# Kernel optimization log

Measured on AMD Instinct MI355X. Metric: run time of the kernel, lower is better.

The kernel has to match this reference:

```python
import jax, jax.numpy as jnp
import numpy as np

L = 512
Z_DIM = 128
C = 128
EPS = 1e-5


def _ln(x, g, b):
    m = jnp.mean(x, axis=-1, keepdims=True)
    v = jnp.var(x, axis=-1, keepdims=True)
    return (x - m) * jax.lax.rsqrt(v + EPS) * g + b


def setup_inputs() -> dict:
    key = jax.random.key(0)
    ks = jax.random.split(key, 12)
    s_z = 1.0 / np.sqrt(Z_DIM)
    s_c = 1.0 / np.sqrt(C)
    return {
        "z": jax.random.normal(ks[0], (L, L, Z_DIM), dtype=jnp.float32),
        "norm_g": jnp.ones((Z_DIM,), jnp.float32),
        "norm_b": jnp.zeros((Z_DIM,), jnp.float32),
        "a_w": jax.random.normal(ks[1], (C, Z_DIM), jnp.float32) * s_z,
        "a_b": jnp.zeros((C,), jnp.float32),
        "ag_w": jax.random.normal(ks[2], (C, Z_DIM), jnp.float32) * s_z,
        "ag_b": jnp.zeros((C,), jnp.float32),
        "onorm_g": jnp.ones((C,), jnp.float32),
        "onorm_b": jnp.zeros((C,), jnp.float32),
        "o_w": jax.random.normal(ks[3], (Z_DIM, C), jnp.float32) * s_c,
        "o_b": jnp.zeros((Z_DIM,), jnp.float32),
        "g_w": jax.random.normal(ks[4], (Z_DIM, Z_DIM), jnp.float32) * s_z,
        "g_b": jnp.zeros((Z_DIM,), jnp.float32),
    }


def reference(z, norm_g, norm_b, a_w, a_b, ag_w, ag_b, onorm_g, onorm_b, o_w, o_b, g_w, g_b):
    zn = _ln(z, norm_g, norm_b)                                   # [L, L, z_dim]
    # gated projection; source computes b identically to a (alinear/aglinear for both)
    a = (zn @ a_w.T + a_b) * jax.nn.sigmoid(zn @ ag_w.T + ag_b)   # [L, L, c]
    o = jnp.einsum('ilc,jlc->ijc', a, a)                          # [L, L, c]
    o = _ln(o, onorm_g, onorm_b)
    o = o @ o_w.T + o_b                                           # [L, L, z_dim]
    return o * jax.nn.sigmoid(zn @ g_w.T + g_b)
```

## Files before the change

### kernel.cpp

```cpp
#include <hip/hip_runtime.h>
#include <stdint.h>

typedef unsigned short bf16;
typedef __attribute__((ext_vector_type(8))) short short8;
typedef __attribute__((ext_vector_type(4))) float f32x4;

#define MFMA16(a, b, c) __builtin_amdgcn_mfma_f32_16x16x32_bf16((a), (b), (c), 0, 0, 0)

__device__ __forceinline__ bf16 f2bf(float f) {
    unsigned u = __float_as_uint(f);
    u += 0x7fffu + ((u >> 16) & 1u);
    return (bf16)(u >> 16);
}
__device__ __forceinline__ float bf2f(bf16 s) { return __uint_as_float(((unsigned)s) << 16); }

__device__ __forceinline__ void gload_lds16(const void* g, void* lds) {
    auto gp = (const __attribute__((address_space(1))) unsigned int*)(uintptr_t)g;
    auto lp = (__attribute__((address_space(3))) unsigned int*)(uintptr_t)lds;
    __builtin_amdgcn_global_load_lds(gp, lp, 16, 0, 0);
}

__global__ __launch_bounds__(256) void k_wconv(const float* __restrict__ aw,
                                               const float* __restrict__ agw,
                                               const float* __restrict__ gw,
                                               const float* __restrict__ ow,
                                               bf16* __restrict__ wbf,
                                               bf16* __restrict__ owbf) {
    int i = blockIdx.x * 256 + threadIdx.x;
    int m = i >> 14, k = i & 16383;
    const float* s = (m == 0) ? aw : (m == 1) ? agw : (m == 2) ? gw : ow;
    float v = s[k];
    if (m < 3) wbf[i] = f2bf(v); else owbf[k] = f2bf(v);
}

__global__ __launch_bounds__(256) void k_ln_proj(const float* __restrict__ z,
                                                 const float* __restrict__ ng,
                                                 const float* __restrict__ nb,
                                                 const float* __restrict__ ab,
                                                 const float* __restrict__ agb,
                                                 const float* __restrict__ gbv,
                                                 const bf16* __restrict__ wbf,
                                                 bf16* __restrict__ a_t,
                                                 bf16* __restrict__ gbuf) {
    __shared__ bf16 zn_s[64 * 136];
    __shared__ bf16 w_s[128 * 136];
    __shared__ float ng_s[128], nb_s[128];

    const int t = threadIdx.x;
    const int r0 = blockIdx.x * 64;
    bf16* st = w_s;

    if (t < 128) { ng_s[t] = ng[t]; nb_s[t] = nb[t]; }

    {
        int row = t >> 2, q = t & 3;
        const float* zp = z + (size_t)(r0 + row) * 128 + q * 32;
        float x[32];
        float s = 0.f, ss = 0.f;
#pragma unroll
        for (int i = 0; i < 8; ++i) {
            float4 v = ((const float4*)zp)[i];
            x[4 * i + 0] = v.x; x[4 * i + 1] = v.y; x[4 * i + 2] = v.z; x[4 * i + 3] = v.w;
        }
#pragma unroll
        for (int i = 0; i < 32; ++i) { s += x[i]; ss += x[i] * x[i]; }
        s += __shfl_xor(s, 1); ss += __shfl_xor(ss, 1);
        s += __shfl_xor(s, 2); ss += __shfl_xor(ss, 2);
        float mean = s * (1.f / 128.f);
        float var = ss * (1.f / 128.f) - mean * mean;
        float rstd = rsqrtf(var + 1e-5f);
        __syncthreads();
#pragma unroll
        for (int i = 0; i < 32; ++i) {
            int c = q * 32 + i;
            zn_s[row * 136 + c] = f2bf((x[i] - mean) * rstd * ng_s[c] + nb_s[c]);
        }
    }

    const int lane = t & 63, w = t >> 6;
    const int lr = lane & 15, quad = lane >> 4;
    const int arow = w * 16 + lr;

    auto stage_w = [&](int mat) {
        const uint4* src = (const uint4*)(wbf + mat * 16384);
#pragma unroll
        for (int i = 0; i < 8; ++i) {
            int idx = t + i * 256;
            int row = idx >> 4, part = idx & 15;
            *(uint4*)&w_s[row * 136 + part * 8] = src[idx];
        }
    };
    auto gemmv = [&](f32x4* acc) {
#pragma unroll
        for (int kk = 0; kk < 4; ++kk) {
            short8 af = *(const short8*)&zn_s[arow * 136 + kk * 32 + quad * 8];
#pragma unroll
            for (int nt = 0; nt < 8; ++nt) {
                short8 bfr = *(const short8*)&w_s[(nt * 16 + lr) * 136 + kk * 32 + quad * 8];
                acc[nt] = MFMA16(af, bfr, acc[nt]);
            }
        }
    };

    f32x4 zero4 = {0.f, 0.f, 0.f, 0.f};
    f32x4 acc_a[8], acc_b[8];
#pragma unroll
    for (int nt = 0; nt < 8; ++nt) { acc_a[nt] = zero4; acc_b[nt] = zero4; }

    stage_w(0);
    __syncthreads();
    gemmv(acc_a);
    __syncthreads();
    stage_w(1);
    __syncthreads();
    gemmv(acc_b);
    __syncthreads();

#pragma unroll
    for (int nt = 0; nt < 8; ++nt) {
        int c = nt * 16 + lr;
        float abv = ab[c], agbv = agb[c];
#pragma unroll
        for (int r = 0; r < 4; ++r) {
            int row = w * 16 + quad * 4 + r;
            float av = acc_a[nt][r] + abv;
            float agvv = acc_b[nt][r] + agbv;
            st[c * 64 + row] = f2bf(av * (1.f / (1.f + __expf(-agvv))));
        }
    }
    __syncthreads();
#pragma unroll
    for (int i = 0; i < 4; ++i) {
        int idx = t + i * 256;
        int c = idx >> 3, part = idx & 7;
        *(uint4*)(a_t + (size_t)c * 262144 + r0 + part * 8) = *(const uint4*)&st[c * 64 + part * 8];
    }
    __syncthreads();

    stage_w(2);
    __syncthreads();
#pragma unroll
    for (int nt = 0; nt < 8; ++nt) acc_a[nt] = zero4;
    gemmv(acc_a);
    __syncthreads();
#pragma unroll
    for (int nt = 0; nt < 8; ++nt) {
        int c = nt * 16 + lr;
        float gb0 = gbv[c];
#pragma unroll
        for (int r = 0; r < 4; ++r) {
            int row = w * 16 + quad * 4 + r;
            float v = acc_a[nt][r] + gb0;
            st[row * 128 + c] = f2bf(1.f / (1.f + __expf(-v)));
        }
    }
    __syncthreads();
#pragma unroll
    for (int i = 0; i < 4; ++i) {
        int idx = t + i * 256;
        int row = idx >> 4, part = idx & 15;
        *(uint4*)(gbuf + (size_t)(r0 + row) * 128 + part * 8) = *(const uint4*)&st[row * 128 + part * 8];
    }
}

__global__ __launch_bounds__(256) void k_einsum(const bf16* __restrict__ a_t,
                                                bf16* __restrict__ o_t) {
    __shared__ bf16 smem[16384];
    bf16* As = smem;
    bf16* Bs = smem + 8192;

    const int t = threadIdx.x;
    const int bx = blockIdx.x;
    const int c = bx >> 4;
    const int ti = (bx >> 2) & 3, tj = bx & 3;
    const int i0 = ti * 128, j0 = tj * 128;
    const size_t cbase = (size_t)c * 262144;
    const bf16* Ac = a_t + cbase;

    const int lane = t & 63, w = t >> 6;
    const int lr = lane & 15, quad = lane >> 4;
    const int wi = w >> 1, wj = w & 1;

    f32x4 zero4 = {0.f, 0.f, 0.f, 0.f};
    f32x4 acc[4][4];
#pragma unroll
    for (int mt = 0; mt < 4; ++mt)
#pragma unroll
        for (int nt = 0; nt < 4; ++nt) acc[mt][nt] = zero4;

    for (int kb = 0; kb < 8; ++kb) {
        __syncthreads();
#pragma unroll
        for (int q = 0; q < 4; ++q) {
            int t16 = (w << 8) + (q << 6) + lane;
            int row = t16 >> 3;
            int cb = t16 & 7;
            int cbg = cb ^ (row & 7);
            int gcol = kb * 64 + cbg * 8;
            gload_lds16(Ac + (size_t)(i0 + row) * 512 + gcol, As + (((w << 8) + (q << 6)) << 3));
            gload_lds16(Ac + (size_t)(j0 + row) * 512 + gcol, Bs + (((w << 8) + (q << 6)) << 3));
        }
        __syncthreads();
#pragma unroll
        for (int kk8 = 0; kk8 < 8; kk8 += 4) {
            short8 af[4], bfr[4];
#pragma unroll
            for (int mt = 0; mt < 4; ++mt) {
                int r = wi * 64 + mt * 16 + lr;
                af[mt] = *(const short8*)&As[r * 64 + (((kk8 + quad) ^ (lr & 7)) << 3)];
            }
#pragma unroll
            for (int nt = 0; nt < 4; ++nt) {
                int r = wj * 64 + nt * 16 + lr;
                bfr[nt] = *(const short8*)&Bs[r * 64 + (((kk8 + quad) ^ (lr & 7)) << 3)];
            }
#pragma unroll
            for (int mt = 0; mt < 4; ++mt)
#pragma unroll
                for (int nt = 0; nt < 4; ++nt)
                    acc[mt][nt] = MFMA16(af[mt], bfr[nt], acc[mt][nt]);
        }
    }

    __syncthreads();
    bf16* Cs = smem;
#pragma unroll
    for (int mt = 0; mt < 4; ++mt)
#pragma unroll
        for (int nt = 0; nt < 4; ++nt)
#pragma unroll
            for (int r = 0; r < 4; ++r) {
                int il = wi * 64 + mt * 16 + quad * 4 + r;
                int jl = wj * 64 + nt * 16 + lr;
                Cs[il * 128 + jl] = f2bf(acc[mt][nt][r]);
            }
    __syncthreads();
    bf16* Oc = o_t + cbase;
#pragma unroll
    for (int i = 0; i < 8; ++i) {
        int idx = t + (i << 8);
        int row = idx >> 4, part = idx & 15;
        *(uint4*)(Oc + (size_t)(i0 + row) * 512 + j0 + part * 8) = *(const uint4*)&Cs[row * 128 + part * 8];
    }
}

__global__ __launch_bounds__(256) void k_out(const bf16* __restrict__ o_t,
                                             const bf16* __restrict__ gbuf,
                                             const float* __restrict__ og,
                                             const float* __restrict__ ob,
                                             const bf16* __restrict__ owbf,
                                             const float* __restrict__ obias,
                                             float* __restrict__ out) {
    __shared__ bf16 pool[128 * 136];
    __shared__ float og_s[128], ob_s[128], obi_s[128];
    bf16* ot_s = pool;
    bf16* n_s = pool;

    const int t = threadIdx.x;
    const int p0 = blockIdx.x * 128;
    if (t < 128) { og_s[t] = og[t]; ob_s[t] = ob[t]; obi_s[t] = obias[t]; }

#pragma unroll
    for (int i = 0; i < 8; ++i) {
        int idx = t + (i << 8);
        int c = idx >> 4, part = idx & 15;
        *(uint4*)&ot_s[c * 128 + part * 8] = *(const uint4*)(o_t + (size_t)c * 262144 + p0 + part * 8);
    }
    __syncthreads();

    {
        int col = t >> 1, h = t & 1;
        float s = 0.f, ss = 0.f;
        float xv[64];
#pragma unroll
        for (int k = 0; k < 64; ++k) {
            float x = bf2f(ot_s[(h * 64 + k) * 128 + col]);
            xv[k] = x; s += x; ss += x * x;
        }
        s += __shfl_xor(s, 1); ss += __shfl_xor(ss, 1);
        float mean = s * (1.f / 128.f);
        float var = ss * (1.f / 128.f) - mean * mean;
        float rstd = rsqrtf(var + 1e-5f);
        __syncthreads();
#pragma unroll
        for (int k = 0; k < 64; ++k) {
            int cc = h * 64 + k;
            n_s[col * 136 + cc] = f2bf((xv[k] - mean) * rstd * og_s[cc] + ob_s[cc]);
        }
    }
    __syncthreads();

    const int lane = t & 63, w = t >> 6;
    const int lr = lane & 15, quad = lane >> 4;
    f32x4 zero4 = {0.f, 0.f, 0.f, 0.f};
    f32x4 acc[2][8];
#pragma unroll
    for (int mt = 0; mt < 2; ++mt)
#pragma unroll
        for (int nt = 0; nt < 8; ++nt) acc[mt][nt] = zero4;

#pragma unroll
    for (int kk = 0; kk < 4; ++kk) {
        short8 af[2];
#pragma unroll
        for (int mt = 0; mt < 2; ++mt)
            af[mt] = *(const short8*)&n_s[(w * 32 + mt * 16 + lr) * 136 + kk * 32 + quad * 8];
#pragma unroll
        for (int nt = 0; nt < 8; ++nt) {
            short8 bfr = *(const short8*)(owbf + (nt * 16 + lr) * 128 + kk * 32 + quad * 8);
            acc[0][nt] = MFMA16(af[0], bfr, acc[0][nt]);
            acc[1][nt] = MFMA16(af[1], bfr, acc[1][nt]);
        }
    }

#pragma unroll
    for (int mt = 0; mt < 2; ++mt)
#pragma unroll
        for (int nt = 0; nt < 8; ++nt) {
            int zd = nt * 16 + lr;
            float bias = obi_s[zd];
#pragma unroll
            for (int r = 0; r < 4; ++r) {
                int m = w * 32 + mt * 16 + quad * 4 + r;
                size_t off = (size_t)(p0 + m) * 128 + zd;
                out[off] = (acc[mt][nt][r] + bias) * bf2f(gbuf[off]);
            }
        }
}

extern "C" void kernel_launch(void* const* d_in, const int* in_sizes, int n_in,
                              void* d_out, int out_size, void* d_ws, size_t ws_size,
                              hipStream_t stream) {
    (void)in_sizes; (void)n_in; (void)out_size; (void)ws_size;
    const float* z   = (const float*)d_in[0];
    const float* ng  = (const float*)d_in[1];
    const float* nb  = (const float*)d_in[2];
    const float* aw  = (const float*)d_in[3];
    const float* ab  = (const float*)d_in[4];
    const float* agw = (const float*)d_in[5];
    const float* agb = (const float*)d_in[6];
    const float* ong = (const float*)d_in[7];
    const float* onb = (const float*)d_in[8];
    const float* ow  = (const float*)d_in[9];
    const float* obi = (const float*)d_in[10];
    const float* gw  = (const float*)d_in[11];
    const float* gbb = (const float*)d_in[12];

    char* ws = (char*)d_ws;
    bf16* wbf  = (bf16*)(ws);
    bf16* owbf = (bf16*)(ws + 98304);
    bf16* a_t  = (bf16*)(ws + 131072);
    bf16* gbuf = (bf16*)(ws + 131072 + 67108864);
    bf16* o_t  = (bf16*)(ws + 131072 + 2 * 67108864);

    k_wconv<<<256, 256, 0, stream>>>(aw, agw, gw, ow, wbf, owbf);
    k_ln_proj<<<4096, 256, 0, stream>>>(z, ng, nb, ab, agb, gbb, wbf, a_t, gbuf);
    k_einsum<<<2048, 256, 0, stream>>>(a_t, o_t);
    k_out<<<2048, 256, 0, stream>>>(o_t, gbuf, ong, onb, owbf, obi, (float*)d_out);
}
```

Baseline: 423.2 us.

## Prepack projection weights into MFMA fragment order and load them directly from global

The weight-conversion kernel now writes the three projection weights pre-permuted into the per-lane MFMA B-fragment layout. The LN/projection kernel reads those fragments straight from global (L2-resident) memory instead of staging each weight matrix through LDS with barriers. LDS use drops from about 50KB to about 34KB and several __syncthreads are removed, which should raise occupancy and cut staging overhead. The cost is more global/L2 traffic per block for weight fragments, and latency the MFMA loop has to hide.

Result: slower. 433.8 us (+2.5%).

```diff
diff --git a/kernel.cpp b/kernel.cpp
--- a/kernel.cpp
+++ b/kernel.cpp
@@ -24,13 +24,21 @@
                                                const float* __restrict__ agw,
                                                const float* __restrict__ gw,
                                                const float* __restrict__ ow,
-                                               bf16* __restrict__ wbf,
+                                               bf16* __restrict__ wpk,
                                                bf16* __restrict__ owbf) {
     int i = blockIdx.x * 256 + threadIdx.x;
-    int m = i >> 14, k = i & 16383;
-    const float* s = (m == 0) ? aw : (m == 1) ? agw : (m == 2) ? gw : ow;
-    float v = s[k];
-    if (m < 3) wbf[i] = f2bf(v); else owbf[k] = f2bf(v);
+    if (i < 49152) {
+        int m = i >> 14, r = i & 16383;
+        int kk = r >> 12, rr = r & 4095;
+        int nt = rr >> 9, li = rr & 511;
+        int lane = li >> 3, e = li & 7;
+        int lr = lane & 15, quad = lane >> 4;
+        const float* s = (m == 0) ? aw : (m == 1) ? agw : gw;
+        wpk[i] = f2bf(s[(nt * 16 + lr) * 128 + kk * 32 + quad * 8 + e]);
+    } else {
+        int k = i - 49152;
+        owbf[k] = f2bf(ow[k]);
+    }
 }
 
 __global__ __launch_bounds__(256) void k_ln_proj(const float* __restrict__ z,
@@ -39,16 +47,15 @@
                                                  const float* __restrict__ ab,
                                                  const float* __restrict__ agb,
                                                  const float* __restrict__ gbv,
-                                                 const bf16* __restrict__ wbf,
+                                                 const bf16* __restrict__ wpk,
                                                  bf16* __restrict__ a_t,
                                                  bf16* __restrict__ gbuf) {
     __shared__ bf16 zn_s[64 * 136];
-    __shared__ bf16 w_s[128 * 136];
+    __shared__ bf16 st[8192];
     __shared__ float ng_s[128], nb_s[128];
 
     const int t = threadIdx.x;
     const int r0 = blockIdx.x * 64;
-    bf16* st = w_s;
 
     if (t < 128) { ng_s[t] = ng[t]; nb_s[t] = nb[t]; }
 
@@ -76,45 +83,30 @@
             zn_s[row * 136 + c] = f2bf((x[i] - mean) * rstd * ng_s[c] + nb_s[c]);
         }
     }
+    __syncthreads();
 
     const int lane = t & 63, w = t >> 6;
     const int lr = lane & 15, quad = lane >> 4;
     const int arow = w * 16 + lr;
 
-    auto stage_w = [&](int mat) {
-        const uint4* src = (const uint4*)(wbf + mat * 16384);
-#pragma unroll
-        for (int i = 0; i < 8; ++i) {
-            int idx = t + i * 256;
-            int row = idx >> 4, part = idx & 15;
-            *(uint4*)&w_s[row * 136 + part * 8] = src[idx];
-        }
-    };
-    auto gemmv = [&](f32x4* acc) {
-#pragma unroll
-        for (int kk = 0; kk < 4; ++kk) {
-            short8 af = *(const short8*)&zn_s[arow * 136 + kk * 32 + quad * 8];
-#pragma unroll
-            for (int nt = 0; nt < 8; ++nt) {
-                short8 bfr = *(const short8*)&w_s[(nt * 16 + lr) * 136 + kk * 32 + quad * 8];
-                acc[nt] = MFMA16(af, bfr, acc[nt]);
-            }
-        }
-    };
+    const short8* w0 = (const short8*)wpk + lane;
+    const short8* w1 = (const short8*)(wpk + 16384) + lane;
+    const short8* w2 = (const short8*)(wpk + 32768) + lane;
 
     f32x4 zero4 = {0.f, 0.f, 0.f, 0.f};
     f32x4 acc_a[8], acc_b[8];
 #pragma unroll
     for (int nt = 0; nt < 8; ++nt) { acc_a[nt] = zero4; acc_b[nt] = zero4; }
 
-    stage_w(0);
-    __syncthreads();
-    gemmv(acc_a);
-    __syncthreads();
-    stage_w(1);
-    __syncthreads();
-    gemmv(acc_b);
-    __syncthreads();
+#pragma unroll
+    for (int kk = 0; kk < 4; ++kk) {
+        short8 af = *(const short8*)&zn_s[arow * 136 + kk * 32 + quad * 8];
+#pragma unroll
+        for (int nt = 0; nt < 8; ++nt) {
+            acc_a[nt] = MFMA16(af, w0[(kk * 8 + nt) * 64], acc_a[nt]);
+            acc_b[nt] = MFMA16(af, w1[(kk * 8 + nt) * 64], acc_b[nt]);
+        }
+    }
 
 #pragma unroll
     for (int nt = 0; nt < 8; ++nt) {
@@ -129,20 +121,25 @@
         }
     }
     __syncthreads();
+
 #pragma unroll
     for (int i = 0; i < 4; ++i) {
         int idx = t + i * 256;
         int c = idx >> 3, part = idx & 7;
         *(uint4*)(a_t + (size_t)c * 262144 + r0 + part * 8) = *(const uint4*)&st[c * 64 + part * 8];
     }
-    __syncthreads();
-
-    stage_w(2);
-    __syncthreads();
+
 #pragma unroll
     for (int nt = 0; nt < 8; ++nt) acc_a[nt] = zero4;
-    gemmv(acc_a);
-    __syncthreads();
+#pragma unroll
+    for (int kk = 0; kk < 4; ++kk) {
+        short8 af = *(const short8*)&zn_s[arow * 136 + kk * 32 + quad * 8];
+#pragma unroll
+        for (int nt = 0; nt < 8; ++nt)
+            acc_a[nt] = MFMA16(af, w2[(kk * 8 + nt) * 64], acc_a[nt]);
+    }
+    __syncthreads();
+
 #pragma unroll
     for (int nt = 0; nt < 8; ++nt) {
         int c = nt * 16 + lr;
@@ -155,6 +152,7 @@
         }
     }
     __syncthreads();
+
 #pragma unroll
     for (int i = 0; i < 4; ++i) {
         int idx = t + i * 256;
@@ -347,14 +345,14 @@
     const float* gbb = (const float*)d_in[12];
 
     char* ws = (char*)d_ws;
-    bf16* wbf  = (bf16*)(ws);
+    bf16* wpk  = (bf16*)(ws);
     bf16* owbf = (bf16*)(ws + 98304);
     bf16* a_t  = (bf16*)(ws + 131072);
     bf16* gbuf = (bf16*)(ws + 131072 + 67108864);
     bf16* o_t  = (bf16*)(ws + 131072 + 2 * 67108864);
 
-    k_wconv<<<256, 256, 0, stream>>>(aw, agw, gw, ow, wbf, owbf);
-    k_ln_proj<<<4096, 256, 0, stream>>>(z, ng, nb, ab, agb, gbb, wbf, a_t, gbuf);
+    k_wconv<<<256, 256, 0, stream>>>(aw, agw, gw, ow, wpk, owbf);
+    k_ln_proj<<<4096, 256, 0, stream>>>(z, ng, nb, ab, agb, gbb, wpk, a_t, gbuf);
     k_einsum<<<2048, 256, 0, stream>>>(a_t, o_t);
     k_out<<<2048, 256, 0, stream>>>(o_t, gbuf, ong, onb, owbf, obi, (float*)d_out);
 }
```
